# Kernel optimization log

Hardware: AMD Instinct MI355X
Metric: run time of the kernel (lower is better)

## Reference

```python
import jax, jax.numpy as jnp
import numpy as np

LN_EPS = 1e-5


def _ln(x, g, b):
    m = jnp.mean(x, axis=-1, keepdims=True)
    v = jnp.mean((x - m) ** 2, axis=-1, keepdims=True)
    return (x - m) / jnp.sqrt(v + LN_EPS) * g + b


def setup_inputs() -> dict:
    key = jax.random.key(0)
    ks = jax.random.split(key, 8)
    B, N, S, D, T = 16, 64, 2048, 1024, 768

    def xavier(k, shape):
        fan_in, fan_out = shape
        lim = (6.0 / (fan_in + fan_out)) ** 0.5
        return jax.random.uniform(k, shape, minval=-lim, maxval=lim, dtype=jnp.float32)

    return {
        "prev_states": jax.random.normal(ks[0], (B, N, D), dtype=jnp.float32),
        "input_tokens": jax.random.normal(ks[1], (B, S, T), dtype=jnp.float32),
        # input_projection (token_dim -> state_dim)
        "W_proj": xavier(ks[2], (T, D)),
        "b_proj": jnp.zeros((D,), jnp.float32),
        # three LayerNorms
        "g_state": jnp.ones((D,), jnp.float32), "beta_state": jnp.zeros((D,), jnp.float32),
        "g_input": jnp.ones((D,), jnp.float32), "beta_input": jnp.zeros((D,), jnp.float32),
        "g_out": jnp.ones((D,), jnp.float32), "beta_out": jnp.zeros((D,), jnp.float32),
        # GRU gates (2D -> D); update-gate bias initialized to -1 as in the module
        "W_u": xavier(ks[3], (2 * D, D)), "b_u": jnp.full((D,), -1.0, jnp.float32),
        "W_r": xavier(ks[4], (2 * D, D)), "b_r": jnp.zeros((D,), jnp.float32),
        "W_n": xavier(ks[5], (2 * D, D)), "b_n": jnp.zeros((D,), jnp.float32),
    }


def reference(prev_states, input_tokens, W_proj, b_proj,
              g_state, beta_state, g_input, beta_input, g_out, beta_out,
              W_u, b_u, W_r, b_r, W_n, b_n):
    D = prev_states.shape[-1]
    # project tokens to state dim: (B,S,D)
    tok = input_tokens @ W_proj + b_proj
    # attention routing (routing_weights=None path)
    scores = jnp.einsum('bnd,bsd->bns', prev_states, tok) / jnp.sqrt(jnp.float32(D))
    attn = jax.nn.softmax(scores, axis=-1)
    routed = jnp.einsum('bns,bsd->bnd', attn, tok)  # (B,N,D)
    # GRU-style gated update, vectorized over the num_states axis
    ps_n = _ln(prev_states, g_state, beta_state)
    in_n = _ln(routed, g_input, beta_input)
    concat = jnp.concatenate([ps_n, in_n], axis=-1)  # (B,N,2D)
    u = jax.nn.sigmoid(concat @ W_u + b_u)
    r = jax.nn.sigmoid(concat @ W_r + b_r)
    reset_in = jnp.concatenate([r * ps_n, in_n], axis=-1)
    cand = jnp.tanh(reset_in @ W_n + b_n)  # dropout is identity in eval
    new_state = (1.0 - u) * prev_states + u * cand
    return _ln(new_state, g_out, beta_out)
```

## Files before the change

### kernel.cpp

```cpp
#include <hip/hip_runtime.h>
#include <stdint.h>

typedef __attribute__((ext_vector_type(4))) float floatx4;
typedef __attribute__((ext_vector_type(8))) short shortx8;

#define LN_EPS 1e-5f

__device__ __forceinline__ unsigned short f2b(float f) {
  unsigned u = __builtin_bit_cast(unsigned, f);
  u = (u + 0x7FFFu + ((u >> 16) & 1u)) >> 16;
  return (unsigned short)u;
}
__device__ __forceinline__ float b2f(unsigned short h) {
  return __builtin_bit_cast(float, (unsigned)h << 16);
}

__device__ __forceinline__ void g2l16(const unsigned short* g, unsigned short* l) {
  __builtin_amdgcn_global_load_lds(
      (const __attribute__((address_space(1))) unsigned int*)g,
      (__attribute__((address_space(3))) unsigned int*)l, 16, 0, 0);
}

__device__ __forceinline__ float wave_sum(float v) {
#pragma unroll
  for (int o = 32; o; o >>= 1) v += __shfl_down(v, o, 64);
  return v;
}
__device__ __forceinline__ float block_sum(float v, float* s) {
  v = wave_sum(v);
  __syncthreads();
  if ((threadIdx.x & 63) == 0) s[threadIdx.x >> 6] = v;
  __syncthreads();
  return s[0] + s[1] + s[2] + s[3];
}

__global__ __launch_bounds__(256) void k_prep(
    const float* __restrict__ prev, unsigned short* __restrict__ psb,
    const float* __restrict__ wp, unsigned short* __restrict__ wpb,
    const float* __restrict__ Wu, const float* __restrict__ Wr,
    const float* __restrict__ Wn,
    unsigned short* __restrict__ Wtur, unsigned short* __restrict__ Wtn,
    unsigned short* __restrict__ Wtp, float* __restrict__ rs) {
  __shared__ float tile[32][33];
  const int bid = blockIdx.x;
  if (bid < 896) {
    if (bid == 0) {
      floatx4 z = {0.f, 0.f, 0.f, 0.f};
      *(floatx4*)(rs + threadIdx.x * 4) = z;
    }
    const float* src;
    unsigned short* dst;
    long i;
    if (bid < 512) { src = prev; dst = psb; i = ((long)bid * 256 + threadIdx.x) * 8; }
    else { src = wp; dst = wpb; i = ((long)(bid - 512) * 256 + threadIdx.x) * 8; }
    floatx4 v0 = *(const floatx4*)(src + i);
    floatx4 v1 = *(const floatx4*)(src + i + 4);
    unsigned short t8[8];
#pragma unroll
    for (int j = 0; j < 4; j++) { t8[j] = f2b(v0[j]); t8[4 + j] = f2b(v1[j]); }
    *(uint4*)(dst + i) = *(uint4*)t8;
    return;
  }
  int t = bid - 896;
  const float* in;
  unsigned short* out;
  int K, kx, ny;
  if (t < 6144) {
    const int which = t >> 11;
    const int t2 = t & 2047;
    kx = t2 & 63;
    ny = t2 >> 6;
    K = 2048;
    in = which == 0 ? Wu : (which == 1 ? Wr : Wn);
    out = which == 0 ? Wtur : (which == 1 ? Wtur + 1024 * 2048 : Wtn);
  } else {
    const int t2 = t - 6144;
    kx = t2 % 24;
    ny = t2 / 24;
    K = 768;
    in = wp;
    out = Wtp;
  }
  const int N = 1024;
  const int k0 = kx * 32, n0 = ny * 32;
  const int tx = threadIdx.x & 31, ty = threadIdx.x >> 5;
#pragma unroll
  for (int i = 0; i < 32; i += 8)
    tile[ty + i][tx] = in[(long)(k0 + ty + i) * N + n0 + tx];
  __syncthreads();
#pragma unroll
  for (int i = 0; i < 32; i += 8)
    out[(long)(n0 + ty + i) * K + k0 + tx] = f2b(tile[tx][ty + i]);
}

__global__ __launch_bounds__(256) void k_gemm64(
    const unsigned short* __restrict__ A, int lda,
    const unsigned short* __restrict__ Bt, int ldb,
    int K,
    const float* __restrict__ bias, const float* __restrict__ bias2,
    int mode,
    void* __restrict__ out, int ldc,
    unsigned short* __restrict__ out2,
    const unsigned short* __restrict__ aux_psn,
    const float* __restrict__ aux_u, const float* __restrict__ aux_prev) {
  __shared__ unsigned short As[2][64 * 64];
  __shared__ unsigned short Bs[2][64 * 64];
  const int tid = threadIdx.x;
  const int wave = tid >> 6, lane = tid & 63;
  const int flat = blockIdx.x + blockIdx.y * gridDim.x;
  const int q = (gridDim.x * gridDim.y) >> 3;
  const int swz = (flat & 7) * q + (flat >> 3);
  const int m0 = (swz % gridDim.x) * 64;
  const int n0 = (swz / gridDim.x) * 64;
  const int wm = wave & 1, wn = wave >> 1;
  const int l16 = lane & 15, quad = lane >> 4;
  const int srow8 = lane >> 3;
  const int c8 = ((lane & 7) ^ srow8) * 8;

  const unsigned short* gA[2];
  const unsigned short* gB[2];
  int lOff[2];
#pragma unroll
  for (int j = 0; j < 2; j++) {
    const int rb = wave * 16 + j * 8;
    gA[j] = A + (long)(m0 + rb + srow8) * lda + c8;
    gB[j] = Bt + (long)(n0 + rb + srow8) * ldb + c8;
    lOff[j] = rb * 64;
  }
  int offA[2][2], offB[2][2];
#pragma unroll
  for (int ks = 0; ks < 2; ks++)
#pragma unroll
    for (int i = 0; i < 2; i++) {
      int r = wm * 32 + i * 16 + l16;
      offA[ks][i] = r * 64 + (((ks * 4 + quad) ^ (r & 7)) * 8);
      r = wn * 32 + i * 16 + l16;
      offB[ks][i] = r * 64 + (((ks * 4 + quad) ^ (r & 7)) * 8);
    }

  floatx4 acc[2][2] = {};

#pragma unroll
  for (int j = 0; j < 2; j++) {
    g2l16(gA[j], &As[0][lOff[j]]);
    g2l16(gB[j], &Bs[0][lOff[j]]);
  }
  __syncthreads();

  const int nt = K >> 6;
  for (int t = 0; t < nt; t++) {
    const int cur = t & 1;
    if (t + 1 < nt) {
      const int kn = (t + 1) << 6;
#pragma unroll
      for (int j = 0; j < 2; j++) {
        g2l16(gA[j] + kn, &As[cur ^ 1][lOff[j]]);
        g2l16(gB[j] + kn, &Bs[cur ^ 1][lOff[j]]);
      }
    }
#pragma unroll
    for (int ks = 0; ks < 2; ks++) {
      shortx8 af[2], bf[2];
#pragma unroll
      for (int i = 0; i < 2; i++) af[i] = *(const shortx8*)&As[cur][offA[ks][i]];
#pragma unroll
      for (int j = 0; j < 2; j++) bf[j] = *(const shortx8*)&Bs[cur][offB[ks][j]];
#pragma unroll
      for (int i = 0; i < 2; i++)
#pragma unroll
        for (int j = 0; j < 2; j++)
          acc[i][j] = __builtin_amdgcn_mfma_f32_16x16x32_bf16(af[i], bf[j], acc[i][j], 0, 0, 0);
    }
    __syncthreads();
  }

#pragma unroll
  for (int i = 0; i < 2; i++)
#pragma unroll
    for (int j = 0; j < 2; j++) {
      const int rbase = m0 + wm * 32 + i * 16 + quad * 4;
      const int c = n0 + wn * 32 + j * 16 + l16;
      float bval = 0.0f;
      if (bias) bval = (mode == 5 && c >= 1024) ? bias2[c - 1024] : bias[c];
#pragma unroll
      for (int r = 0; r < 4; r++) {
        const int row = rbase + r;
        float v = acc[i][j][r] + bval;
        if (mode == 1) {
          out2[(long)row * ldc + c] = f2b(v);
        } else if (mode == 3) {
          float cand = tanhf(v);
          float u = aux_u[(long)row * 1024 + c];
          float p = aux_prev[(long)row * 1024 + c];
          ((float*)out)[(long)row * ldc + c] = (1.0f - u) * p + u * cand;
        } else if (mode == 6) {
          ((float*)out)[(long)row * ldc + c] = v + aux_u[row] * bias2[c];
        } else {
          if (c < 1024) {
            ((float*)out)[(long)row * 1024 + c] = 1.0f / (1.0f + expf(-v));
          } else {
            const int cc = c - 1024;
            float rr = 1.0f / (1.0f + expf(-v));
            out2[(long)row * 2048 + cc] = f2b(rr * b2f(aux_psn[(long)row * 2048 + cc]));
          }
        }
      }
    }
}

__global__ __launch_bounds__(256) void k_scores(
    const unsigned short* __restrict__ A, long sAb, int lda,
    const float* __restrict__ toksf,
    int K, float scale,
    unsigned short* __restrict__ out2, int ldc, long sCb,
    float* __restrict__ rs) {
  __shared__ unsigned short As[2][64 * 64];
  __shared__ unsigned short Bs[2][64 * 64];
  const int tid = threadIdx.x;
  const int wave = tid >> 6, lane = tid & 63;
  const int b = blockIdx.z;
  const int m0 = 0, n0 = blockIdx.y * 64;
  const int wm = wave & 1, wn = wave >> 1;
  const int l16 = lane & 15, quad = lane >> 4;
  const int srow8 = lane >> 3;
  const int c8 = ((lane & 7) ^ srow8) * 8;
  const unsigned short* Ab = A + (long)b * sAb;

  const unsigned short* gA[2];
  const float* gBf[2];
  int lOff[2];
#pragma unroll
  for (int j = 0; j < 2; j++) {
    const int rb = wave * 16 + j * 8;
    gA[j] = Ab + (long)(m0 + rb + srow8) * lda + c8;
    gBf[j] = toksf + (long)b * 1572864 + (long)(n0 + rb + srow8) * 768 + c8;
    lOff[j] = rb * 64;
  }
  int offA[2][2], offB[2][2];
#pragma unroll
  for (int ks = 0; ks < 2; ks++)
#pragma unroll
    for (int i = 0; i < 2; i++) {
      int r = wm * 32 + i * 16 + l16;
      offA[ks][i] = r * 64 + (((ks * 4 + quad) ^ (r & 7)) * 8);
      r = wn * 32 + i * 16 + l16;
      offB[ks][i] = r * 64 + (((ks * 4 + quad) ^ (r & 7)) * 8);
    }

  floatx4 acc[2][2] = {};

#pragma unroll
  for (int j = 0; j < 2; j++) {
    g2l16(gA[j], &As[0][lOff[j]]);
    floatx4 v0 = *(const floatx4*)(gBf[j]);
    floatx4 v1 = *(const floatx4*)(gBf[j] + 4);
    unsigned short t8[8];
#pragma unroll
    for (int i = 0; i < 4; i++) { t8[i] = f2b(v0[i]); t8[4 + i] = f2b(v1[i]); }
    *(uint4*)&Bs[0][lOff[j] + lane * 8] = *(uint4*)t8;
  }
  __syncthreads();

  const int nt = K >> 6;
  for (int t = 0; t < nt; t++) {
    const int cur = t & 1;
    floatx4 w0[2], w1[2];
    if (t + 1 < nt) {
      const int kn = (t + 1) << 6;
#pragma unroll
      for (int j = 0; j < 2; j++) {
        g2l16(gA[j] + kn, &As[cur ^ 1][lOff[j]]);
        w0[j] = *(const floatx4*)(gBf[j] + kn);
        w1[j] = *(const floatx4*)(gBf[j] + kn + 4);
      }
    }
#pragma unroll
    for (int ks = 0; ks < 2; ks++) {
      shortx8 af[2], bf[2];
#pragma unroll
      for (int i = 0; i < 2; i++) af[i] = *(const shortx8*)&As[cur][offA[ks][i]];
#pragma unroll
      for (int j = 0; j < 2; j++) bf[j] = *(const shortx8*)&Bs[cur][offB[ks][j]];
#pragma unroll
      for (int i = 0; i < 2; i++)
#pragma unroll
        for (int j = 0; j < 2; j++)
          acc[i][j] = __builtin_amdgcn_mfma_f32_16x16x32_bf16(af[i], bf[j], acc[i][j], 0, 0, 0);
    }
    if (t + 1 < nt) {
#pragma unroll
      for (int j = 0; j < 2; j++) {
        unsigned short t8[8];
#pragma unroll
        for (int i = 0; i < 4; i++) { t8[i] = f2b(w0[j][i]); t8[4 + i] = f2b(w1[j][i]); }
        *(uint4*)&Bs[cur ^ 1][lOff[j] + lane * 8] = *(uint4*)t8;
      }
    }
    __syncthreads();
  }

#pragma unroll
  for (int i = 0; i < 2; i++) {
    float psum[4] = {0.f, 0.f, 0.f, 0.f};
#pragma unroll
    for (int j = 0; j < 2; j++) {
      const int rbase = m0 + wm * 32 + i * 16 + quad * 4;
      const int c = n0 + wn * 32 + j * 16 + l16;
#pragma unroll
      for (int r = 0; r < 4; r++) {
        const float e = expf(acc[i][j][r] * scale);
        out2[(long)b * sCb + (long)(rbase + r) * ldc + c] = f2b(e);
        psum[r] += e;
      }
    }
#pragma unroll
    for (int r = 0; r < 4; r++) {
      float s = psum[r];
      s += __shfl_xor(s, 1, 64);
      s += __shfl_xor(s, 2, 64);
      s += __shfl_xor(s, 4, 64);
      s += __shfl_xor(s, 8, 64);
      if (l16 == 0)
        atomicAdd(rs + (long)b * 64 + m0 + wm * 32 + i * 16 + quad * 4 + r, s);
    }
  }
}

__global__ __launch_bounds__(256) void k_routed_mfma(
    const unsigned short* __restrict__ attnb,
    const float* __restrict__ tokf,
    float* __restrict__ parts) {
  __shared__ unsigned short As[64 * 40];
  __shared__ unsigned short Bs[32 * 66];
  const int kc = blockIdx.x, nt = blockIdx.y, b = blockIdx.z;
  const int tid = threadIdx.x;
  const int wave = tid >> 6, lane = tid & 63;
  const int wm = wave & 1, wn = wave >> 1;
  const int l16 = lane & 15, quad = lane >> 4;
  const int n0 = nt * 64;
  const long abase = (long)b * 131072 + (long)kc * 1024;
  const long tbase = ((long)b * 2048 + (long)kc * 1024) * 768;
  const int srow = tid >> 2, skc = (tid & 3) * 8;
  const int bk = tid >> 3, bd = (tid & 7) * 8;

  floatx4 acc[2][2] = {};

  uint4 pa = *(const uint4*)(attnb + abase + (long)srow * 2048 + skc);
  floatx4 f0 = *(const floatx4*)(tokf + tbase + (long)bk * 768 + n0 + bd);
  floatx4 f1 = *(const floatx4*)(tokf + tbase + (long)bk * 768 + n0 + bd + 4);

  for (int k0 = 0; k0 < 1024; k0 += 32) {
    *(uint4*)&As[srow * 40 + skc] = pa;
    {
      unsigned short t8[8];
#pragma unroll
      for (int i = 0; i < 4; i++) { t8[i] = f2b(f0[i]); t8[4 + i] = f2b(f1[i]); }
      unsigned short* dst = &Bs[bk * 66 + bd];
#pragma unroll
      for (int w2 = 0; w2 < 4; w2++) *(unsigned*)(dst + w2 * 2) = ((unsigned*)t8)[w2];
    }
    if (k0 + 32 < 1024) {
      pa = *(const uint4*)(attnb + abase + (long)srow * 2048 + (k0 + 32) + skc);
      f0 = *(const floatx4*)(tokf + tbase + (long)(k0 + 32 + bk) * 768 + n0 + bd);
      f1 = *(const floatx4*)(tokf + tbase + (long)(k0 + 32 + bk) * 768 + n0 + bd + 4);
    }
    asm volatile("s_waitcnt lgkmcnt(0)" ::: "memory");
    __builtin_amdgcn_s_barrier();
    __builtin_amdgcn_sched_barrier(0);

    shortx8 a0 = *(const shortx8*)&As[(wm * 32 + 0  + l16) * 40 + quad * 8];
    shortx8 a1 = *(const shortx8*)&As[(wm * 32 + 16 + l16) * 40 + quad * 8];
    shortx8 b0, b1;
#pragma unroll
    for (int j = 0; j < 8; j++) {
      b0[j] = *(const short*)&Bs[(quad * 8 + j) * 66 + wn * 32 + l16];
      b1[j] = *(const short*)&Bs[(quad * 8 + j) * 66 + wn * 32 + 16 + l16];
    }
    acc[0][0] = __builtin_amdgcn_mfma_f32_16x16x32_bf16(a0, b0, acc[0][0], 0, 0, 0);
    acc[0][1] = __builtin_amdgcn_mfma_f32_16x16x32_bf16(a0, b1, acc[0][1], 0, 0, 0);
    acc[1][0] = __builtin_amdgcn_mfma_f32_16x16x32_bf16(a1, b0, acc[1][0], 0, 0, 0);
    acc[1][1] = __builtin_amdgcn_mfma_f32_16x16x32_bf16(a1, b1, acc[1][1], 0, 0, 0);
    __builtin_amdgcn_s_barrier();
  }

#pragma unroll
  for (int im = 0; im < 2; im++)
#pragma unroll
    for (int in_ = 0; in_ < 2; in_++) {
      const int rbase = wm * 32 + im * 16 + quad * 4;
      const int c = n0 + wn * 32 + in_ * 16 + l16;
#pragma unroll
      for (int r = 0; r < 4; r++)
        parts[(long)kc * 786432 + ((long)b * 64 + rbase + r) * 768 + c] =
            acc[im][in_][r];
    }
}

__global__ __launch_bounds__(256) void k_sumcvt(
    const float* __restrict__ parts, unsigned short* __restrict__ out) {
  const long i = ((long)blockIdx.x * 256 + threadIdx.x) * 4;
  floatx4 v = *(const floatx4*)(parts + i);
  floatx4 w = *(const floatx4*)(parts + 786432 + i);
  unsigned short t4[4];
#pragma unroll
  for (int j = 0; j < 4; j++) t4[j] = f2b(v[j] + w[j]);
  *(uint2*)(out + i) = *(uint2*)t4;
}

__global__ __launch_bounds__(256) void k_ln2(
    const float* __restrict__ prev, const float* __restrict__ routed,
    const float* __restrict__ g_st, const float* __restrict__ be_st,
    const float* __restrict__ g_in, const float* __restrict__ be_in,
    unsigned short* __restrict__ conc, unsigned short* __restrict__ candA) {
  __shared__ float scr[4];
  const long r = blockIdx.x & 1023;
  const bool second = blockIdx.x >= 1024;
  const int t = threadIdx.x;
  floatx4 v;
  const float *g, *be;
  if (!second) {
    v = *(const floatx4*)(prev + r * 1024 + t * 4);
    g = g_st; be = be_st;
  } else {
    v = *(const floatx4*)(routed + r * 1024 + t * 4);
    g = g_in; be = be_in;
  }
  float s1 = v[0] + v[1] + v[2] + v[3];
  float s2 = v[0] * v[0] + v[1] * v[1] + v[2] * v[2] + v[3] * v[3];
  s1 = block_sum(s1, scr);
  s2 = block_sum(s2, scr);
  const float mean = s1 * (1.0f / 1024.0f);
  const float var = s2 * (1.0f / 1024.0f) - mean * mean;
  const float rstd = rsqrtf(var + LN_EPS);
#pragma unroll
  for (int i = 0; i < 4; i++) {
    const int d = t * 4 + i;
    const float y = (v[i] - mean) * rstd * g[d] + be[d];
    const unsigned short h = f2b(y);
    if (!second) {
      conc[r * 2048 + d] = h;
    } else {
      conc[r * 2048 + 1024 + d] = h;
      candA[r * 2048 + 1024 + d] = h;
    }
  }
}

__global__ __launch_bounds__(256) void k_ln_out(
    const float* __restrict__ in, const float* __restrict__ g,
    const float* __restrict__ be, float* __restrict__ out) {
  __shared__ float scr[4];
  const long r = blockIdx.x;
  const int t = threadIdx.x;
  floatx4 v = *(const floatx4*)(in + r * 1024 + t * 4);
  float s1 = v[0] + v[1] + v[2] + v[3];
  float s2 = v[0] * v[0] + v[1] * v[1] + v[2] * v[2] + v[3] * v[3];
  s1 = block_sum(s1, scr);
  s2 = block_sum(s2, scr);
  const float mean = s1 * (1.0f / 1024.0f);
  const float var = s2 * (1.0f / 1024.0f) - mean * mean;
  const float rstd = rsqrtf(var + LN_EPS);
  floatx4 o;
#pragma unroll
  for (int i = 0; i < 4; i++) {
    const int d = t * 4 + i;
    o[i] = (v[i] - mean) * rstd * g[d] + be[d];
  }
  *(floatx4*)(out + r * 1024 + t * 4) = o;
}

extern "C" void kernel_launch(void* const* d_in, const int* in_sizes, int n_in,
                              void* d_out, int out_size, void* d_ws, size_t ws_size,
                              hipStream_t stream) {
  (void)in_sizes; (void)n_in; (void)out_size; (void)ws_size;
  const float* prev  = (const float*)d_in[0];
  const float* toks  = (const float*)d_in[1];
  const float* Wp    = (const float*)d_in[2];
  const float* bp    = (const float*)d_in[3];
  const float* g_st  = (const float*)d_in[4];
  const float* be_st = (const float*)d_in[5];
  const float* g_in  = (const float*)d_in[6];
  const float* be_in = (const float*)d_in[7];
  const float* g_o   = (const float*)d_in[8];
  const float* be_o  = (const float*)d_in[9];
  const float* Wu    = (const float*)d_in[10];
  const float* bu    = (const float*)d_in[11];
  const float* Wr    = (const float*)d_in[12];
  const float* br    = (const float*)d_in[13];
  const float* Wn    = (const float*)d_in[14];
  const float* bn    = (const float*)d_in[15];
  float* out = (float*)d_out;

  char* ws = (char*)d_ws;
  unsigned short* psb   = (unsigned short*)ws; ws += 2097152;
  unsigned short* Wpb   = (unsigned short*)ws; ws += 1572864;
  unsigned short* Wtp   = (unsigned short*)ws; ws += 1572864;
  unsigned short* pwb   = (unsigned short*)ws; ws += 1572864;
  unsigned short* attnb = (unsigned short*)ws; ws += 4194304;
  float*          rowsum= (float*)ws;          ws += 4096;
  float*          parts = (float*)ws;          ws += 6291456;
  unsigned short* rwb   = (unsigned short*)ws; ws += 1572864;
  float*          routed= (float*)ws;          ws += 4194304;
  unsigned short* conc  = (unsigned short*)ws; ws += 4194304;
  unsigned short* candA = (unsigned short*)ws; ws += 4194304;
  float*          ubuf  = (float*)ws;          ws += 4194304;
  float*          ns    = (float*)ws;          ws += 4194304;
  unsigned short* Wtur  = (unsigned short*)ws; ws += 8388608;
  unsigned short* Wtn   = (unsigned short*)ws; ws += 4194304;

  const dim3 blk(256);

  k_prep<<<dim3(7808), blk, 0, stream>>>(prev, psb, Wp, Wpb,
                                         Wu, Wr, Wn, Wtur, Wtn, Wtp, rowsum);
  k_gemm64<<<dim3(16, 12), blk, 0, stream>>>(
      psb, 1024, Wpb, 1024, 1024,
      nullptr, nullptr, 1,
      nullptr, 768, pwb, nullptr, nullptr, nullptr);
  k_scores<<<dim3(1, 32, 16), blk, 0, stream>>>(
      pwb, 49152L, 768, toks, 768, 0.03125f,
      attnb, 2048, 131072L, rowsum);
  k_routed_mfma<<<dim3(2, 12, 16), blk, 0, stream>>>(attnb, toks, parts);
  k_sumcvt<<<dim3(768), blk, 0, stream>>>(parts, rwb);
  k_gemm64<<<dim3(16, 16), blk, 0, stream>>>(
      rwb, 768, Wtp, 768, 768,
      nullptr, bp, 6,
      (void*)routed, 1024, nullptr, nullptr, rowsum, nullptr);
  k_ln2<<<dim3(2048), blk, 0, stream>>>(prev, routed, g_st, be_st, g_in, be_in,
                                        conc, candA);
  k_gemm64<<<dim3(16, 32), blk, 0, stream>>>(
      conc, 2048, Wtur, 2048, 2048,
      bu, br, 5,
      (void*)ubuf, 1024, candA, conc, nullptr, nullptr);
  k_gemm64<<<dim3(16, 16), blk, 0, stream>>>(
      candA, 2048, Wtn, 2048, 2048,
      bn, nullptr, 3,
      (void*)ns, 1024, nullptr, nullptr, ubuf, prev);
  k_ln_out<<<dim3(1024), blk, 0, stream>>>(ns, g_o, be_o, out);
}
```

Baseline: 322.2 us.

## Split-K the gate GEMMs and fuse partial-sum reduction into the A-loads

The two GRU gate GEMMs (K=2048) now run split-K in two halves via blockIdx.z, writing fp32 partials. Separate epilogue kernels reduce those partials: one applies the u/r sigmoids, the other applies tanh and the GRU blend inside the output LayerNorm. The routed-projection GEMM now reads the two fp32 split partials directly, sums them and converts to bf16 while filling LDS, which removes the standalone sumcvt kernel. The goal is more blocks on small-M GEMMs for better CU occupancy, paid for with extra partial-buffer traffic and an added epilogue launch.

```diff
diff --git a/kernel.cpp b/kernel.cpp
--- a/kernel.cpp
+++ b/kernel.cpp
@@ -96,13 +96,120 @@
 __global__ __launch_bounds__(256) void k_gemm64(
     const unsigned short* __restrict__ A, int lda,
     const unsigned short* __restrict__ Bt, int ldb,
-    int K,
+    int K, long sCk,
     const float* __restrict__ bias, const float* __restrict__ bias2,
     int mode,
     void* __restrict__ out, int ldc,
     unsigned short* __restrict__ out2,
-    const unsigned short* __restrict__ aux_psn,
-    const float* __restrict__ aux_u, const float* __restrict__ aux_prev) {
+    const unsigned short* __restrict__ aux_psn) {
+  __shared__ unsigned short As[2][64 * 64];
+  __shared__ unsigned short Bs[2][64 * 64];
+  const int tid = threadIdx.x;
+  const int wave = tid >> 6, lane = tid & 63;
+  const int kc = blockIdx.z;
+  const long koff = (long)kc * K;
+  const int flat = blockIdx.x + blockIdx.y * gridDim.x;
+  const int q = (gridDim.x * gridDim.y) >> 3;
+  const int swz = (flat & 7) * q + (flat >> 3);
+  const int m0 = (swz % gridDim.x) * 64;
+  const int n0 = (swz / gridDim.x) * 64;
+  const int wm = wave & 1, wn = wave >> 1;
+  const int l16 = lane & 15, quad = lane >> 4;
+  const int srow8 = lane >> 3;
+  const int c8 = ((lane & 7) ^ srow8) * 8;
+
+  const unsigned short* gA[2];
+  const unsigned short* gB[2];
+  int lOff[2];
+#pragma unroll
+  for (int j = 0; j < 2; j++) {
+    const int rb = wave * 16 + j * 8;
+    gA[j] = A + (long)(m0 + rb + srow8) * lda + c8 + koff;
+    gB[j] = Bt + (long)(n0 + rb + srow8) * ldb + c8 + koff;
+    lOff[j] = rb * 64;
+  }
+  int offA[2][2], offB[2][2];
+#pragma unroll
+  for (int ks = 0; ks < 2; ks++)
+#pragma unroll
+    for (int i = 0; i < 2; i++) {
+      int r = wm * 32 + i * 16 + l16;
+      offA[ks][i] = r * 64 + (((ks * 4 + quad) ^ (r & 7)) * 8);
+      r = wn * 32 + i * 16 + l16;
+      offB[ks][i] = r * 64 + (((ks * 4 + quad) ^ (r & 7)) * 8);
+    }
+
+  floatx4 acc[2][2] = {};
+
+#pragma unroll
+  for (int j = 0; j < 2; j++) {
+    g2l16(gA[j], &As[0][lOff[j]]);
+    g2l16(gB[j], &Bs[0][lOff[j]]);
+  }
+  __syncthreads();
+
+  const int nt = K >> 6;
+  for (int t = 0; t < nt; t++) {
+    const int cur = t & 1;
+    if (t + 1 < nt) {
+      const int kn = (t + 1) << 6;
+#pragma unroll
+      for (int j = 0; j < 2; j++) {
+        g2l16(gA[j] + kn, &As[cur ^ 1][lOff[j]]);
+        g2l16(gB[j] + kn, &Bs[cur ^ 1][lOff[j]]);
+      }
+    }
+#pragma unroll
+    for (int ks = 0; ks < 2; ks++) {
+      shortx8 af[2], bf[2];
+#pragma unroll
+      for (int i = 0; i < 2; i++) af[i] = *(const shortx8*)&As[cur][offA[ks][i]];
+#pragma unroll
+      for (int j = 0; j < 2; j++) bf[j] = *(const shortx8*)&Bs[cur][offB[ks][j]];
+#pragma unroll
+      for (int i = 0; i < 2; i++)
+#pragma unroll
+        for (int j = 0; j < 2; j++)
+          acc[i][j] = __builtin_amdgcn_mfma_f32_16x16x32_bf16(af[i], bf[j], acc[i][j], 0, 0, 0);
+    }
+    __syncthreads();
+  }
+
+#pragma unroll
+  for (int i = 0; i < 2; i++)
+#pragma unroll
+    for (int j = 0; j < 2; j++) {
+      const int rbase = m0 + wm * 32 + i * 16 + quad * 4;
+      const int c = n0 + wn * 32 + j * 16 + l16;
+      float bval = 0.0f;
+      if (bias) bval = (mode == 5 && c >= 1024) ? bias2[c - 1024] : bias[c];
+#pragma unroll
+      for (int r = 0; r < 4; r++) {
+        const int row = rbase + r;
+        float v = acc[i][j][r] + bval;
+        if (mode == 1) {
+          out2[(long)row * ldc + c] = f2b(v);
+        } else if (mode == 7) {
+          ((float*)out)[(long)kc * sCk + (long)row * ldc + c] = v;
+        } else {
+          if (c < 1024) {
+            ((float*)out)[(long)row * 1024 + c] = 1.0f / (1.0f + expf(-v));
+          } else {
+            const int cc = c - 1024;
+            float rr = 1.0f / (1.0f + expf(-v));
+            out2[(long)row * 2048 + cc] = f2b(rr * b2f(aux_psn[(long)row * 2048 + cc]));
+          }
+        }
+      }
+    }
+}
+
+__global__ __launch_bounds__(256) void k_gemm64_af32(
+    const float* __restrict__ P0, int lda,
+    const unsigned short* __restrict__ Bt, int ldb,
+    int K,
+    const float* __restrict__ bp, const float* __restrict__ rowsum,
+    float* __restrict__ out, int ldc) {
   __shared__ unsigned short As[2][64 * 64];
   __shared__ unsigned short Bs[2][64 * 64];
   const int tid = threadIdx.x;
@@ -117,13 +224,13 @@
   const int srow8 = lane >> 3;
   const int c8 = ((lane & 7) ^ srow8) * 8;
 
-  const unsigned short* gA[2];
+  const float* gAf[2];
   const unsigned short* gB[2];
   int lOff[2];
 #pragma unroll
   for (int j = 0; j < 2; j++) {
     const int rb = wave * 16 + j * 8;
-    gA[j] = A + (long)(m0 + rb + srow8) * lda + c8;
+    gAf[j] = P0 + (long)(m0 + rb + srow8) * lda + c8;
     gB[j] = Bt + (long)(n0 + rb + srow8) * ldb + c8;
     lOff[j] = rb * 64;
   }
@@ -142,20 +249,31 @@
 
 #pragma unroll
   for (int j = 0; j < 2; j++) {
-    g2l16(gA[j], &As[0][lOff[j]]);
     g2l16(gB[j], &Bs[0][lOff[j]]);
+    floatx4 a0 = *(const floatx4*)(gAf[j]);
+    floatx4 a1 = *(const floatx4*)(gAf[j] + 4);
+    floatx4 b0 = *(const floatx4*)(gAf[j] + 786432);
+    floatx4 b1 = *(const floatx4*)(gAf[j] + 786432 + 4);
+    unsigned short t8[8];
+#pragma unroll
+    for (int i = 0; i < 4; i++) { t8[i] = f2b(a0[i] + b0[i]); t8[4 + i] = f2b(a1[i] + b1[i]); }
+    *(uint4*)&As[0][lOff[j] + lane * 8] = *(uint4*)t8;
   }
   __syncthreads();
 
   const int nt = K >> 6;
   for (int t = 0; t < nt; t++) {
     const int cur = t & 1;
+    floatx4 a0[2], a1[2], p0[2], p1[2];
     if (t + 1 < nt) {
       const int kn = (t + 1) << 6;
 #pragma unroll
       for (int j = 0; j < 2; j++) {
-        g2l16(gA[j] + kn, &As[cur ^ 1][lOff[j]]);
         g2l16(gB[j] + kn, &Bs[cur ^ 1][lOff[j]]);
+        a0[j] = *(const floatx4*)(gAf[j] + kn);
+        a1[j] = *(const floatx4*)(gAf[j] + kn + 4);
+        p0[j] = *(const floatx4*)(gAf[j] + kn + 786432);
+        p1[j] = *(const floatx4*)(gAf[j] + kn + 786432 + 4);
       }
     }
 #pragma unroll
@@ -170,6 +288,18 @@
 #pragma unroll
         for (int j = 0; j < 2; j++)
           acc[i][j] = __builtin_amdgcn_mfma_f32_16x16x32_bf16(af[i], bf[j], acc[i][j], 0, 0, 0);
+    }
+    if (t + 1 < nt) {
+#pragma unroll
+      for (int j = 0; j < 2; j++) {
+        unsigned short t8[8];
+#pragma unroll
+        for (int i = 0; i < 4; i++) {
+          t8[i] = f2b(a0[j][i] + p0[j][i]);
+          t8[4 + i] = f2b(a1[j][i] + p1[j][i]);
+        }
+        *(uint4*)&As[cur ^ 1][lOff[j] + lane * 8] = *(uint4*)t8;
+      }
     }
     __syncthreads();
   }
@@ -180,30 +310,10 @@
     for (int j = 0; j < 2; j++) {
       const int rbase = m0 + wm * 32 + i * 16 + quad * 4;
       const int c = n0 + wn * 32 + j * 16 + l16;
-      float bval = 0.0f;
-      if (bias) bval = (mode == 5 && c >= 1024) ? bias2[c - 1024] : bias[c];
 #pragma unroll
       for (int r = 0; r < 4; r++) {
         const int row = rbase + r;
-        float v = acc[i][j][r] + bval;
-        if (mode == 1) {
-          out2[(long)row * ldc + c] = f2b(v);
-        } else if (mode == 3) {
-          float cand = tanhf(v);
-          float u = aux_u[(long)row * 1024 + c];
-          float p = aux_prev[(long)row * 1024 + c];
-          ((float*)out)[(long)row * ldc + c] = (1.0f - u) * p + u * cand;
-        } else if (mode == 6) {
-          ((float*)out)[(long)row * ldc + c] = v + aux_u[row] * bias2[c];
-        } else {
-          if (c < 1024) {
-            ((float*)out)[(long)row * 1024 + c] = 1.0f / (1.0f + expf(-v));
-          } else {
-            const int cc = c - 1024;
-            float rr = 1.0f / (1.0f + expf(-v));
-            out2[(long)row * 2048 + cc] = f2b(rr * b2f(aux_psn[(long)row * 2048 + cc]));
-          }
-        }
+        out[(long)row * ldc + c] = acc[i][j][r] + rowsum[row] * bp[c];
       }
     }
 }
@@ -396,17 +506,6 @@
     }
 }
 
-__global__ __launch_bounds__(256) void k_sumcvt(
-    const float* __restrict__ parts, unsigned short* __restrict__ out) {
-  const long i = ((long)blockIdx.x * 256 + threadIdx.x) * 4;
-  floatx4 v = *(const floatx4*)(parts + i);
-  floatx4 w = *(const floatx4*)(parts + 786432 + i);
-  unsigned short t4[4];
-#pragma unroll
-  for (int j = 0; j < 4; j++) t4[j] = f2b(v[j] + w[j]);
-  *(uint2*)(out + i) = *(uint2*)t4;
-}
-
 __global__ __launch_bounds__(256) void k_ln2(
     const float* __restrict__ prev, const float* __restrict__ routed,
     const float* __restrict__ g_st, const float* __restrict__ be_st,
@@ -446,13 +545,56 @@
   }
 }
 
+__global__ __launch_bounds__(256) void k_gate_epi(
+    const float* __restrict__ gparts,
+    const float* __restrict__ bu, const float* __restrict__ br,
+    const unsigned short* __restrict__ conc,
+    float* __restrict__ ubuf, unsigned short* __restrict__ candA) {
+  const int row = blockIdx.x >> 1;
+  const int half = blockIdx.x & 1;
+  const int t = threadIdx.x;
+  const long base = (long)row * 2048 + half * 1024 + t * 4;
+  floatx4 p0 = *(const floatx4*)(gparts + base);
+  floatx4 p1 = *(const floatx4*)(gparts + 2097152 + base);
+  const float* bias = half ? br : bu;
+  floatx4 bv = *(const floatx4*)(bias + t * 4);
+  if (!half) {
+    floatx4 o;
+#pragma unroll
+    for (int i = 0; i < 4; i++)
+      o[i] = 1.0f / (1.0f + expf(-(p0[i] + p1[i] + bv[i])));
+    *(floatx4*)(ubuf + (long)row * 1024 + t * 4) = o;
+  } else {
+    unsigned short t4[4];
+#pragma unroll
+    for (int i = 0; i < 4; i++) {
+      float rr = 1.0f / (1.0f + expf(-(p0[i] + p1[i] + bv[i])));
+      t4[i] = f2b(rr * b2f(conc[(long)row * 2048 + t * 4 + i]));
+    }
+    *(uint2*)(candA + (long)row * 2048 + t * 4) = *(uint2*)t4;
+  }
+}
+
 __global__ __launch_bounds__(256) void k_ln_out(
-    const float* __restrict__ in, const float* __restrict__ g,
-    const float* __restrict__ be, float* __restrict__ out) {
+    const float* __restrict__ cparts,
+    const float* __restrict__ ubuf, const float* __restrict__ prev,
+    const float* __restrict__ bn,
+    const float* __restrict__ g, const float* __restrict__ be,
+    float* __restrict__ out) {
   __shared__ float scr[4];
   const long r = blockIdx.x;
   const int t = threadIdx.x;
-  floatx4 v = *(const floatx4*)(in + r * 1024 + t * 4);
+  floatx4 p0 = *(const floatx4*)(cparts + r * 1024 + t * 4);
+  floatx4 p1 = *(const floatx4*)(cparts + 1048576 + r * 1024 + t * 4);
+  floatx4 uu = *(const floatx4*)(ubuf + r * 1024 + t * 4);
+  floatx4 pv = *(const floatx4*)(prev + r * 1024 + t * 4);
+  floatx4 bv = *(const floatx4*)(bn + t * 4);
+  floatx4 v;
+#pragma unroll
+  for (int i = 0; i < 4; i++) {
+    const float cand = tanhf(p0[i] + p1[i] + bv[i]);
+    v[i] = (1.0f - uu[i]) * pv[i] + uu[i] * cand;
+  }
   float s1 = v[0] + v[1] + v[2] + v[3];
   float s2 = v[0] * v[0] + v[1] * v[1] + v[2] * v[2] + v[3] * v[3];
   s1 = block_sum(s1, scr);
@@ -499,41 +641,39 @@
   unsigned short* attnb = (unsigned short*)ws; ws += 4194304;
   float*          rowsum= (float*)ws;          ws += 4096;
   float*          parts = (float*)ws;          ws += 6291456;
-  unsigned short* rwb   = (unsigned short*)ws; ws += 1572864;
   float*          routed= (float*)ws;          ws += 4194304;
   unsigned short* conc  = (unsigned short*)ws; ws += 4194304;
   unsigned short* candA = (unsigned short*)ws; ws += 4194304;
   float*          ubuf  = (float*)ws;          ws += 4194304;
-  float*          ns    = (float*)ws;          ws += 4194304;
   unsigned short* Wtur  = (unsigned short*)ws; ws += 8388608;
   unsigned short* Wtn   = (unsigned short*)ws; ws += 4194304;
+  float*          gparts= (float*)ws;          ws += 16777216;
+  float*          cparts= (float*)ws;          ws += 8388608;
 
   const dim3 blk(256);
 
   k_prep<<<dim3(7808), blk, 0, stream>>>(prev, psb, Wp, Wpb,
                                          Wu, Wr, Wn, Wtur, Wtn, Wtp, rowsum);
-  k_gemm64<<<dim3(16, 12), blk, 0, stream>>>(
-      psb, 1024, Wpb, 1024, 1024,
+  k_gemm64<<<dim3(16, 12, 1), blk, 0, stream>>>(
+      psb, 1024, Wpb, 1024, 1024, 0L,
       nullptr, nullptr, 1,
-      nullptr, 768, pwb, nullptr, nullptr, nullptr);
+      nullptr, 768, pwb, nullptr);
   k_scores<<<dim3(1, 32, 16), blk, 0, stream>>>(
       pwb, 49152L, 768, toks, 768, 0.03125f,
       attnb, 2048, 131072L, rowsum);
   k_routed_mfma<<<dim3(2, 12, 16), blk, 0, stream>>>(attnb, toks, parts);
-  k_sumcvt<<<dim3(768), blk, 0, stream>>>(parts, rwb);
-  k_gemm64<<<dim3(16, 16), blk, 0, stream>>>(
-      rwb, 768, Wtp, 768, 768,
-      nullptr, bp, 6,
-      (void*)routed, 1024, nullptr, nullptr, rowsum, nullptr);
+  k_gemm64_af32<<<dim3(16, 16), blk, 0, stream>>>(
+      parts, 768, Wtp, 768, 768, bp, rowsum, routed, 1024);
   k_ln2<<<dim3(2048), blk, 0, stream>>>(prev, routed, g_st, be_st, g_in, be_in,
                                         conc, candA);
-  k_gemm64<<<dim3(16, 32), blk, 0, stream>>>(
-      conc, 2048, Wtur, 2048, 2048,
-      bu, br, 5,
-      (void*)ubuf, 1024, candA, conc, nullptr, nullptr);
-  k_gemm64<<<dim3(16, 16), blk, 0, stream>>>(
-      candA, 2048, Wtn, 2048, 2048,
-      bn, nullptr, 3,
-      (void*)ns, 1024, nullptr, nullptr, ubuf, prev);
-  k_ln_out<<<dim3(1024), blk, 0, stream>>>(ns, g_o, be_o, out);
-}
+  k_gemm64<<<dim3(16, 32, 2), blk, 0, stream>>>(
+      conc, 2048, Wtur, 2048, 1024, 2097152L,
+      nullptr, nullptr, 7,
+      (void*)gparts, 2048, nullptr, nullptr);
+  k_gate_epi<<<dim3(2048), blk, 0, stream>>>(gparts, bu, br, conc, ubuf, candA);
+  k_gemm64<<<dim3(16, 16, 2), blk, 0, stream>>>(
+      candA, 2048, Wtn, 2048, 1024, 1048576L,
+      nullptr, nullptr, 7,
+      (void*)cparts, 1024, nullptr, nullptr);
+  k_ln_out<<<dim3(1024), blk, 0, stream>>>(cparts, ubuf, prev, bn, g_o, be_o, out);
+}
```

New measurement: 305.5 us. 5.2% less time.
